# Performance work log

Measured on AMD Instinct MI355X. Metric: run time of the kernel, lower is better.

## Reference

```python
import jax, jax.numpy as jnp
import numpy as np

N = 4000      # number_of_sensors
D_IN = 128    # input feature dim
D_OUT = 128   # output feature dim
E_DIM = 16    # node embedding dim
B = 8         # batch size


def setup_inputs() -> dict:
    key = jax.random.key(0)
    k_x, k_e1, k_e2, k_w = jax.random.split(key, 4)
    x = jax.random.normal(k_x, (B, N, D_IN), dtype=jnp.float32)
    E1 = jax.random.normal(k_e1, (N, E_DIM), dtype=jnp.float32)
    E2 = jax.random.normal(k_e2, (N, E_DIM), dtype=jnp.float32)
    W = jax.random.normal(k_w, (D_IN, D_OUT), dtype=jnp.float32) * (1.0 / np.sqrt(D_IN))
    b = jnp.zeros((D_OUT,), dtype=jnp.float32)
    return {"x": x, "E1": E1, "E2": E2, "W": W, "b": b}


def reference(x, E1, E2, W, b):
    # Adaptive adjacency from node embeddings: A = softmax(relu(E1 @ E2^T), axis=-1)
    logits = jax.nn.relu(jnp.einsum('nd,md->nm', E1, E2))  # [N, N]
    adj = jax.nn.softmax(logits, axis=-1)                  # row-normalized adjacency
    # Graph aggregation then feature transform: relu(A @ X @ W + b)
    agg = jnp.einsum('nm,bmf->bnf', adj, x)                # [B, N, D_IN]
    out = jax.nn.relu(jnp.einsum('bnf,fo->bno', agg, W) + b)  # [B, N, D_OUT]
    return out
```

## Files before the change

### kernel.cpp

```cpp
#include <hip/hip_runtime.h>
#include <hip/hip_bf16.h>

#define NSEN 4000
#define NP   4096
#define DIN  128
#define DOUT 128
#define EDIM 16
#define BATCH 8

typedef __attribute__((ext_vector_type(8))) short bf16x8;
typedef __attribute__((ext_vector_type(4))) float f32x4;

__device__ __forceinline__ unsigned short f2bf(float f) {
  unsigned int u = __float_as_uint(f);
  unsigned int r = (u + 0x7FFFu + ((u >> 16) & 1u)) >> 16;
  return (unsigned short)r;
}
__device__ __forceinline__ float bf2f(unsigned short s) {
  unsigned int u = ((unsigned int)s) << 16;
  return __uint_as_float(u);
}

__device__ __forceinline__ void gl_lds16(const void* g, void* l) {
  __builtin_amdgcn_global_load_lds((const __attribute__((address_space(1))) void*)g,
                                   (__attribute__((address_space(3))) void*)l, 16, 0, 0);
}

__global__ __launch_bounds__(512) void k_prep(const float* __restrict__ E1,
                                              const float* __restrict__ E2,
                                              const float* __restrict__ W,
                                              const float* __restrict__ x,
                                              unsigned short* __restrict__ adjp,
                                              float* __restrict__ rinv,
                                              unsigned short* __restrict__ yt) {
  __shared__ float rsum[8][16];
  __shared__ unsigned short wlds[128 * 136];
  const int bx = blockIdx.x;
  const int tid = threadIdx.x;
  const int lane = tid & 63, wv = tid >> 6;
  const int lr = lane & 15, lq = lane >> 4;

  if (bx >= 250) {
    {
      const int fr = tid >> 5;
      const int o4 = tid & 31;
#pragma unroll
      for (int r8 = 0; r8 < 8; r8++) {
        const int f = fr + r8 * 16;
        float4 w4 = *(const float4*)&W[(size_t)f * DOUT + o4 * 4];
        wlds[(o4 * 4 + 0) * 136 + f] = f2bf(w4.x);
        wlds[(o4 * 4 + 1) * 136 + f] = f2bf(w4.y);
        wlds[(o4 * 4 + 2) * 136 + f] = f2bf(w4.z);
        wlds[(o4 * 4 + 3) * 136 + f] = f2bf(w4.w);
      }
    }
    __syncthreads();

    const int yi = bx - 250;
    const int b  = yi >> 4;
    const int m0 = (yi & 15) * 256;
    const int mh = wv >> 2;
    const int os = wv & 3;

    bf16x8 af[2][4];
#pragma unroll
    for (int ot = 0; ot < 2; ot++) {
      const int ob = os * 32 + ot * 16 + lr;
#pragma unroll
      for (int ks = 0; ks < 4; ks++)
        af[ot][ks] = *(const bf16x8*)&wlds[ob * 136 + ks * 32 + lq * 8];
    }

#pragma unroll
    for (int cc = 0; cc < 4; cc++) {
#pragma unroll
      for (int mtile = 0; mtile < 2; mtile++) {
        const int mb = m0 + cc * 64 + mh * 32 + mtile * 16;
        const int m = mb + lr;
        bf16x8 bx8[4];
        if (m < NSEN) {
          const float* xp = &x[((size_t)b * NSEN + m) * DIN + lq * 8];
#pragma unroll
          for (int ks = 0; ks < 4; ks++) {
            float4 v0 = *(const float4*)(xp + ks * 32);
            float4 v1 = *(const float4*)(xp + ks * 32 + 4);
            bx8[ks][0] = (short)f2bf(v0.x); bx8[ks][1] = (short)f2bf(v0.y);
            bx8[ks][2] = (short)f2bf(v0.z); bx8[ks][3] = (short)f2bf(v0.w);
            bx8[ks][4] = (short)f2bf(v1.x); bx8[ks][5] = (short)f2bf(v1.y);
            bx8[ks][6] = (short)f2bf(v1.z); bx8[ks][7] = (short)f2bf(v1.w);
          }
        } else {
#pragma unroll
          for (int ks = 0; ks < 4; ks++)
#pragma unroll
            for (int j = 0; j < 8; j++) bx8[ks][j] = 0;
        }
#pragma unroll
        for (int ot = 0; ot < 2; ot++) {
          f32x4 c = (f32x4){0.f, 0.f, 0.f, 0.f};
#pragma unroll
          for (int ks = 0; ks < 4; ks++)
            c = __builtin_amdgcn_mfma_f32_16x16x32_bf16(af[ot][ks], bx8[ks], c, 0, 0, 0);
#pragma unroll
          for (int i = 0; i < 4; i++)
            yt[(size_t)(b * 128 + os * 32 + ot * 16 + lq * 4 + i) * NP + mb + lr] = f2bf(c[i]);
        }
      }
    }
    return;
  }

  const int n0 = bx * 16;

  float a[8];
  {
    const float* e1p = &E1[(size_t)(n0 + lr) * EDIM + (lq & 1) * 8];
    *(float4*)&a[0] = *(const float4*)e1p;
    *(float4*)&a[4] = *(const float4*)(e1p + 4);
  }
  bf16x8 af1, af2;
#pragma unroll
  for (int j = 0; j < 8; j++) {
    unsigned short hs = f2bf(a[j]);
    af1[j] = (short)hs;
    float lo = a[j] - bf2f(hs);
    af2[j] = (lq < 2) ? (short)f2bf(lo) : (short)0;
  }

  float rs[4] = {0.f, 0.f, 0.f, 0.f};
  for (int t = wv; t < NSEN / 16; t += 8) {
    const int m = t * 16 + lr;
    float bv[8];
    const float* e2p = &E2[(size_t)m * EDIM + (lq & 1) * 8];
    *(float4*)&bv[0] = *(const float4*)e2p;
    *(float4*)&bv[4] = *(const float4*)(e2p + 4);
    bf16x8 bfrag;
#pragma unroll
    for (int j = 0; j < 8; j++) {
      unsigned short hs = f2bf(bv[j]);
      if (lq < 2) bfrag[j] = (short)hs;
      else        bfrag[j] = (short)f2bf(bv[j] - bf2f(hs));
    }
    f32x4 c = (f32x4){0.f, 0.f, 0.f, 0.f};
    c = __builtin_amdgcn_mfma_f32_16x16x32_bf16(af1, bfrag, c, 0, 0, 0);
    c = __builtin_amdgcn_mfma_f32_16x16x32_bf16(af2, bfrag, c, 0, 0, 0);
#pragma unroll
    for (int i = 0; i < 4; i++) {
      float p = __expf(fmaxf(c[i], 0.f));
      rs[i] += p;
      adjp[(size_t)(n0 + lq * 4 + i) * NP + t * 16 + lr] = f2bf(p);
    }
  }
  for (int i = tid; i < 16 * (NP - NSEN); i += 512) {
    int r = i / (NP - NSEN), c = i % (NP - NSEN);
    adjp[(size_t)(n0 + r) * NP + NSEN + c] = 0;
  }
#pragma unroll
  for (int i = 0; i < 4; i++) {
    rs[i] += __shfl_xor(rs[i], 1, 64);
    rs[i] += __shfl_xor(rs[i], 2, 64);
    rs[i] += __shfl_xor(rs[i], 4, 64);
    rs[i] += __shfl_xor(rs[i], 8, 64);
  }
  if (lr == 0) {
#pragma unroll
    for (int i = 0; i < 4; i++) rsum[wv][lq * 4 + i] = rs[i];
  }
  __syncthreads();
  if (tid < 16) {
    float s = 0.f;
#pragma unroll
    for (int w = 0; w < 8; w++) s += rsum[w][tid];
    rinv[n0 + tid] = 1.0f / s;
  }
}

__global__ __launch_bounds__(256, 2) void k_gemm1(const unsigned short* __restrict__ A,
                                                  const unsigned short* __restrict__ Bt,
                                                  unsigned short* __restrict__ part) {
  __shared__ __align__(16) unsigned short smem[32768];
  const int tid = threadIdx.x;
  const int lane = tid & 63, wv = tid >> 6;
  const int wr = wv >> 1, wc = wv & 1;
  const int lr = lane & 15, lq = lane >> 4;
  const int gx = blockIdx.x;
  const int m0 = (gx >> 1) * 128;
  const int kb0 = (gx & 1) * 2048;
  const int b  = blockIdx.y;
  const int c0 = b * 128;
  unsigned short* tA0 = smem;
  unsigned short* tB0 = smem + 16384;

  f32x4 acc[4][4];
#pragma unroll
  for (int p = 0; p < 4; p++)
#pragma unroll
    for (int q = 0; q < 4; q++) acc[p][q] = (f32x4){0.f, 0.f, 0.f, 0.f};

#define STAGE(bufi, kb)                                                              \
  {                                                                                  \
    _Pragma("unroll")                                                                \
    for (int s = 0; s < 4; s++) {                                                    \
      int idx = s * 256 + tid;                                                       \
      int row = idx >> 3;                                                            \
      int kc = ((idx & 7) ^ (row & 7)) << 3;                                         \
      gl_lds16(&A[(size_t)(m0 + row) * NP + (kb) + kc], &tA0[(bufi)*8192 + idx*8]);  \
      gl_lds16(&Bt[(size_t)(c0 + row) * NP + (kb) + kc], &tB0[(bufi)*8192 + idx*8]); \
    }                                                                                \
  }

  STAGE(0, kb0);

  for (int it = 0; it < 32; ++it) {
    const int cur = it & 1;
    if (it < 31) {
      STAGE(cur ^ 1, kb0 + (it + 1) * 64);
      asm volatile("s_waitcnt vmcnt(8)" ::: "memory");
    } else {
      asm volatile("s_waitcnt vmcnt(0)" ::: "memory");
    }
    __builtin_amdgcn_s_barrier();

    bf16x8 af0[4], bf0[4], af1[4], bf1[4];
    {
      const int koff0 = (lq * 8) ^ ((lr & 7) << 3);
#pragma unroll
      for (int p = 0; p < 4; p++)
        af0[p] = *(const bf16x8*)&tA0[cur * 8192 + (wr * 64 + p * 16 + lr) * 64 + koff0];
#pragma unroll
      for (int q = 0; q < 4; q++)
        bf0[q] = *(const bf16x8*)&tB0[cur * 8192 + (wc * 64 + q * 16 + lr) * 64 + koff0];
    }
    __builtin_amdgcn_sched_barrier(0);
    {
      const int koff1 = (32 + lq * 8) ^ ((lr & 7) << 3);
#pragma unroll
      for (int p = 0; p < 4; p++)
        af1[p] = *(const bf16x8*)&tA0[cur * 8192 + (wr * 64 + p * 16 + lr) * 64 + koff1];
#pragma unroll
      for (int q = 0; q < 4; q++)
        bf1[q] = *(const bf16x8*)&tB0[cur * 8192 + (wc * 64 + q * 16 + lr) * 64 + koff1];
    }
    asm volatile("s_waitcnt lgkmcnt(8)" ::: "memory");
    __builtin_amdgcn_sched_barrier(0);
    __builtin_amdgcn_s_setprio(1);
#pragma unroll
    for (int p = 0; p < 4; p++)
#pragma unroll
      for (int q = 0; q < 4; q++)
        acc[p][q] = __builtin_amdgcn_mfma_f32_16x16x32_bf16(af0[p], bf0[q], acc[p][q], 0, 0, 0);
    asm volatile("s_waitcnt lgkmcnt(0)" ::: "memory");
    __builtin_amdgcn_sched_barrier(0);
#pragma unroll
    for (int p = 0; p < 4; p++)
#pragma unroll
      for (int q = 0; q < 4; q++)
        acc[p][q] = __builtin_amdgcn_mfma_f32_16x16x32_bf16(af1[p], bf1[q], acc[p][q], 0, 0, 0);
    __builtin_amdgcn_s_setprio(0);
    __builtin_amdgcn_s_barrier();
  }
#undef STAGE

  const int kh = gx & 1;
  unsigned short* pdst = part + ((size_t)(kh * BATCH + b) * NP + m0) * DIN;
#pragma unroll
  for (int p = 0; p < 4; p++)
#pragma unroll
    for (int q = 0; q < 4; q++) {
      const int col = wc * 64 + q * 16 + lr;
#pragma unroll
      for (int i = 0; i < 4; i++) {
        const int row = wr * 64 + p * 16 + lq * 4 + i;
        pdst[row * DIN + col] = f2bf(acc[p][q][i]);
      }
    }
}

__global__ __launch_bounds__(256) void k_fin(const unsigned short* __restrict__ part,
                                             const float* __restrict__ rinv,
                                             const float* __restrict__ bias,
                                             float* __restrict__ out) {
  const int tid = threadIdx.x;
  const int nl = tid >> 4;
  const int ch = tid & 15;
  const int n  = blockIdx.x * 16 + nl;
  const int b  = blockIdx.y;
  const size_t base = ((size_t)b * NP + n) * DIN + ch * 8;
  const size_t khoff = (size_t)BATCH * NP * DIN;

  bf16x8 p0 = *(const bf16x8*)&part[base];
  bf16x8 p1 = *(const bf16x8*)&part[khoff + base];
  const float rv = rinv[n];
  float4 bb0 = *(const float4*)&bias[ch * 8];
  float4 bb1 = *(const float4*)&bias[ch * 8 + 4];
  float r[8];
#pragma unroll
  for (int j = 0; j < 8; j++) {
    float bbj = (j < 4) ? ((const float*)&bb0)[j] : ((const float*)&bb1)[j - 4];
    r[j] = fmaxf((bf2f((unsigned short)p0[j]) + bf2f((unsigned short)p1[j])) * rv + bbj, 0.f);
  }
  float* op = &out[((size_t)b * NSEN + n) * DOUT + ch * 8];
  *(float4*)op       = make_float4(r[0], r[1], r[2], r[3]);
  *(float4*)(op + 4) = make_float4(r[4], r[5], r[6], r[7]);
}

extern "C" void kernel_launch(void* const* d_in, const int* in_sizes, int n_in,
                              void* d_out, int out_size, void* d_ws, size_t ws_size,
                              hipStream_t stream) {
  const float* x    = (const float*)d_in[0];
  const float* E1   = (const float*)d_in[1];
  const float* E2   = (const float*)d_in[2];
  const float* W    = (const float*)d_in[3];
  const float* bias = (const float*)d_in[4];
  float* out = (float*)d_out;

  char* ws = (char*)d_ws;
  unsigned short* adjp = (unsigned short*)(ws);
  unsigned short* yt   = (unsigned short*)(ws + 33554432);
  float*          rinv = (float*)(ws + 33554432 + 8388608);
  unsigned short* part = (unsigned short*)(ws + 33554432 + 8388608 + 16384);

  k_prep<<<dim3(378), dim3(512), 0, stream>>>(E1, E2, W, x, adjp, rinv, yt);
  k_gemm1<<<dim3(64, BATCH), dim3(256), 0, stream>>>(adjp, yt, part);
  k_fin<<<dim3(250, BATCH), dim3(256), 0, stream>>>(part, rinv, bias, out);
}
```

Before: 77.46 us.

## Fuse split-K reduction and epilogue into GEMM via atomic tile flags

Removes the separate finalize kernel. Each split-K GEMM block writes its bf16 partial tile, then bumps a per-tile atomic counter, and the second block to arrive adds the other partial, scales by the row inverse sum, adds bias, applies ReLU and writes the output. The Y-transform blocks in the prep kernel now stage results in LDS and write them as coalesced 16-byte stores, using smaller 128-row tiles and more blocks. This saves one launch and a full pass over the partials, in exchange for threadfence and atomic synchronization and a larger LDS footprint in the prep kernel.

```diff
diff --git a/kernel.cpp b/kernel.cpp
--- a/kernel.cpp
+++ b/kernel.cpp
@@ -32,9 +32,11 @@
                                               const float* __restrict__ x,
                                               unsigned short* __restrict__ adjp,
                                               float* __restrict__ rinv,
-                                              unsigned short* __restrict__ yt) {
+                                              unsigned short* __restrict__ yt,
+                                              int* __restrict__ flags) {
   __shared__ float rsum[8][16];
   __shared__ unsigned short wlds[128 * 136];
+  __shared__ unsigned short ylds[128 * 136];
   const int bx = blockIdx.x;
   const int tid = threadIdx.x;
   const int lane = tid & 63, wv = tid >> 6;
@@ -57,8 +59,8 @@
     __syncthreads();
 
     const int yi = bx - 250;
-    const int b  = yi >> 4;
-    const int m0 = (yi & 15) * 256;
+    const int b  = yi >> 5;
+    const int m0 = (yi & 31) * 128;
     const int mh = wv >> 2;
     const int os = wv & 3;
 
@@ -72,44 +74,51 @@
     }
 
 #pragma unroll
-    for (int cc = 0; cc < 4; cc++) {
-#pragma unroll
-      for (int mtile = 0; mtile < 2; mtile++) {
-        const int mb = m0 + cc * 64 + mh * 32 + mtile * 16;
-        const int m = mb + lr;
-        bf16x8 bx8[4];
-        if (m < NSEN) {
-          const float* xp = &x[((size_t)b * NSEN + m) * DIN + lq * 8];
-#pragma unroll
-          for (int ks = 0; ks < 4; ks++) {
-            float4 v0 = *(const float4*)(xp + ks * 32);
-            float4 v1 = *(const float4*)(xp + ks * 32 + 4);
-            bx8[ks][0] = (short)f2bf(v0.x); bx8[ks][1] = (short)f2bf(v0.y);
-            bx8[ks][2] = (short)f2bf(v0.z); bx8[ks][3] = (short)f2bf(v0.w);
-            bx8[ks][4] = (short)f2bf(v1.x); bx8[ks][5] = (short)f2bf(v1.y);
-            bx8[ks][6] = (short)f2bf(v1.z); bx8[ks][7] = (short)f2bf(v1.w);
-          }
-        } else {
-#pragma unroll
-          for (int ks = 0; ks < 4; ks++)
-#pragma unroll
-            for (int j = 0; j < 8; j++) bx8[ks][j] = 0;
+    for (int mt = 0; mt < 4; mt++) {
+      const int mloc = mh * 64 + mt * 16;
+      const int m = m0 + mloc + lr;
+      bf16x8 bx8[4];
+      if (m < NSEN) {
+        const float* xp = &x[((size_t)b * NSEN + m) * DIN + lq * 8];
+#pragma unroll
+        for (int ks = 0; ks < 4; ks++) {
+          float4 v0 = *(const float4*)(xp + ks * 32);
+          float4 v1 = *(const float4*)(xp + ks * 32 + 4);
+          bx8[ks][0] = (short)f2bf(v0.x); bx8[ks][1] = (short)f2bf(v0.y);
+          bx8[ks][2] = (short)f2bf(v0.z); bx8[ks][3] = (short)f2bf(v0.w);
+          bx8[ks][4] = (short)f2bf(v1.x); bx8[ks][5] = (short)f2bf(v1.y);
+          bx8[ks][6] = (short)f2bf(v1.z); bx8[ks][7] = (short)f2bf(v1.w);
         }
-#pragma unroll
-        for (int ot = 0; ot < 2; ot++) {
-          f32x4 c = (f32x4){0.f, 0.f, 0.f, 0.f};
-#pragma unroll
-          for (int ks = 0; ks < 4; ks++)
-            c = __builtin_amdgcn_mfma_f32_16x16x32_bf16(af[ot][ks], bx8[ks], c, 0, 0, 0);
-#pragma unroll
-          for (int i = 0; i < 4; i++)
-            yt[(size_t)(b * 128 + os * 32 + ot * 16 + lq * 4 + i) * NP + mb + lr] = f2bf(c[i]);
-        }
-      }
+      } else {
+#pragma unroll
+        for (int ks = 0; ks < 4; ks++)
+#pragma unroll
+          for (int j = 0; j < 8; j++) bx8[ks][j] = 0;
+      }
+#pragma unroll
+      for (int ot = 0; ot < 2; ot++) {
+        f32x4 c = (f32x4){0.f, 0.f, 0.f, 0.f};
+#pragma unroll
+        for (int ks = 0; ks < 4; ks++)
+          c = __builtin_amdgcn_mfma_f32_16x16x32_bf16(af[ot][ks], bx8[ks], c, 0, 0, 0);
+#pragma unroll
+        for (int i = 0; i < 4; i++)
+          ylds[(os * 32 + ot * 16 + lq * 4 + i) * 136 + mloc + lr] = f2bf(c[i]);
+      }
+    }
+    __syncthreads();
+#pragma unroll
+    for (int s2 = 0; s2 < 4; s2++) {
+      int c = s2 * 512 + tid;
+      int row = c >> 4;
+      int mc = c & 15;
+      *(bf16x8*)&yt[(size_t)(b * 128 + row) * NP + m0 + mc * 8] =
+          *(const bf16x8*)&ylds[row * 136 + mc * 8];
     }
     return;
   }
 
+  if (bx == 0 && tid < 256) flags[tid] = 0;
   const int n0 = bx * 16;
 
   float a[8];
@@ -177,7 +186,11 @@
 
 __global__ __launch_bounds__(256, 2) void k_gemm1(const unsigned short* __restrict__ A,
                                                   const unsigned short* __restrict__ Bt,
-                                                  unsigned short* __restrict__ part) {
+                                                  unsigned short* __restrict__ part,
+                                                  int* __restrict__ flags,
+                                                  const float* __restrict__ rinv,
+                                                  const float* __restrict__ bias,
+                                                  float* __restrict__ out) {
   __shared__ __align__(16) unsigned short smem[32768];
   const int tid = threadIdx.x;
   const int lane = tid & 63, wv = tid >> 6;
@@ -262,7 +275,8 @@
 #undef STAGE
 
   const int kh = gx & 1;
-  unsigned short* pdst = part + ((size_t)(kh * BATCH + b) * NP + m0) * DIN;
+  const int tileid = (gx >> 1) * BATCH + b;
+  unsigned short* pdst = part + ((size_t)(kh * 256 + tileid)) * 16384;
 #pragma unroll
   for (int p = 0; p < 4; p++)
 #pragma unroll
@@ -271,37 +285,39 @@
 #pragma unroll
       for (int i = 0; i < 4; i++) {
         const int row = wr * 64 + p * 16 + lq * 4 + i;
-        pdst[row * DIN + col] = f2bf(acc[p][q][i]);
-      }
-    }
-}
-
-__global__ __launch_bounds__(256) void k_fin(const unsigned short* __restrict__ part,
-                                             const float* __restrict__ rinv,
-                                             const float* __restrict__ bias,
-                                             float* __restrict__ out) {
-  const int tid = threadIdx.x;
-  const int nl = tid >> 4;
-  const int ch = tid & 15;
-  const int n  = blockIdx.x * 16 + nl;
-  const int b  = blockIdx.y;
-  const size_t base = ((size_t)b * NP + n) * DIN + ch * 8;
-  const size_t khoff = (size_t)BATCH * NP * DIN;
-
-  bf16x8 p0 = *(const bf16x8*)&part[base];
-  bf16x8 p1 = *(const bf16x8*)&part[khoff + base];
-  const float rv = rinv[n];
-  float4 bb0 = *(const float4*)&bias[ch * 8];
-  float4 bb1 = *(const float4*)&bias[ch * 8 + 4];
-  float r[8];
-#pragma unroll
-  for (int j = 0; j < 8; j++) {
-    float bbj = (j < 4) ? ((const float*)&bb0)[j] : ((const float*)&bb1)[j - 4];
-    r[j] = fmaxf((bf2f((unsigned short)p0[j]) + bf2f((unsigned short)p1[j])) * rv + bbj, 0.f);
-  }
-  float* op = &out[((size_t)b * NSEN + n) * DOUT + ch * 8];
-  *(float4*)op       = make_float4(r[0], r[1], r[2], r[3]);
-  *(float4*)(op + 4) = make_float4(r[4], r[5], r[6], r[7]);
+        pdst[row * 128 + col] = f2bf(acc[p][q][i]);
+      }
+    }
+  __threadfence();
+  __syncthreads();
+  __shared__ int oldv;
+  if (tid == 0) oldv = atomicAdd(&flags[tileid], 1);
+  __syncthreads();
+  if (oldv == 0) return;
+  __threadfence();
+
+  const unsigned short* psrc = part + ((size_t)((kh ^ 1) * 256 + tileid)) * 16384;
+#pragma unroll
+  for (int p = 0; p < 4; p++) {
+    float rv[4];
+#pragma unroll
+    for (int i = 0; i < 4; i++)
+      rv[i] = rinv[m0 + wr * 64 + p * 16 + lq * 4 + i];
+#pragma unroll
+    for (int q = 0; q < 4; q++) {
+      const int col = wc * 64 + q * 16 + lr;
+      const float bb = bias[col];
+#pragma unroll
+      for (int i = 0; i < 4; i++) {
+        const int row = wr * 64 + p * 16 + lq * 4 + i;
+        const int n = m0 + row;
+        if (n < NSEN) {
+          float v = (bf2f(f2bf(acc[p][q][i])) + bf2f(psrc[row * 128 + col])) * rv[i] + bb;
+          out[((size_t)b * NSEN + n) * DOUT + col] = fmaxf(v, 0.f);
+        }
+      }
+    }
+  }
 }
 
 extern "C" void kernel_launch(void* const* d_in, const int* in_sizes, int n_in,
@@ -318,9 +334,9 @@
   unsigned short* adjp = (unsigned short*)(ws);
   unsigned short* yt   = (unsigned short*)(ws + 33554432);
   float*          rinv = (float*)(ws + 33554432 + 8388608);
-  unsigned short* part = (unsigned short*)(ws + 33554432 + 8388608 + 16384);
-
-  k_prep<<<dim3(378), dim3(512), 0, stream>>>(E1, E2, W, x, adjp, rinv, yt);
-  k_gemm1<<<dim3(64, BATCH), dim3(256), 0, stream>>>(adjp, yt, part);
-  k_fin<<<dim3(250, BATCH), dim3(256), 0, stream>>>(part, rinv, bias, out);
-}
+  int*            flags= (int*)(ws + 33554432 + 8388608 + 16384);
+  unsigned short* part = (unsigned short*)(ws + 33554432 + 8388608 + 16384 + 16384);
+
+  k_prep<<<dim3(506), dim3(512), 0, stream>>>(E1, E2, W, x, adjp, rinv, yt, flags);
+  k_gemm1<<<dim3(64, BATCH), dim3(256), 0, stream>>>(adjp, yt, part, flags, rinv, bias, out);
+}
```

Measured after the change: 193.0 us. 2.49x slower.
